# Performance work log

Measured on AMD Instinct MI355X. Metric: run time of the kernel, lower is better.

Reference implementation:

```python
import jax, jax.numpy as jnp
import numpy as np

K = 20           # neighbors
ALPHA = 1.0      # clustering alpha
BN_EPS = 1e-5
NEG_SLOPE = 0.2


def knn_idx(x, k):
    # x: (B, C, N) -> idx (B, N, k) of k nearest neighbors by squared L2
    xx = jnp.sum(x * x, axis=1)                      # (B, N)
    inner = jnp.einsum('bcn,bcm->bnm', x, x)         # (B, N, N)
    pd = -xx[:, :, None] + 2.0 * inner - xx[:, None, :]  # negative sq dist
    return jax.lax.top_k(pd, k)[1]


def graph_feature(x, k):
    # x: (B, C, N) -> (B, 2C, N, k): concat(neighbor - center, center)
    xt = jnp.transpose(x, (0, 2, 1))                 # (B, N, C)
    idx = knn_idx(x, k)                              # (B, N, k)
    feat = jax.vmap(lambda f, i: f[i])(xt, idx)      # (B, N, k, C)
    center = jnp.broadcast_to(xt[:, :, None, :], feat.shape)
    out = jnp.concatenate([feat - center, center], axis=-1)
    return jnp.transpose(out, (0, 3, 1, 2))


def batchnorm(x, g, b, axes):
    # training-mode BN: batch statistics over `axes`, channel axis = 1
    m = jnp.mean(x, axes, keepdims=True)
    v = jnp.var(x, axes, keepdims=True)
    shape = [1] * x.ndim
    shape[1] = x.shape[1]
    return (x - m) / jnp.sqrt(v + BN_EPS) * g.reshape(shape) + b.reshape(shape)


def conv_block2d(x, w, g, b):
    # 1x1 Conv2d (no bias) + BN2d + LeakyReLU; x (B,Cin,N,k), w (Cout,Cin)
    y = jnp.einsum('oc,bcnk->bonk', w, x)
    return jax.nn.leaky_relu(batchnorm(y, g, b, (0, 2, 3)), NEG_SLOPE)


def setup_inputs() -> dict:
    key = jax.random.key(0)
    ks = jax.random.split(key, 16)
    B, C, N = 4, 3, 2048
    d = {
        'x1': jax.random.normal(ks[0], (B, C, N), jnp.float32),
        'x2': jax.random.normal(ks[1], (B, C, N), jnp.float32),
        'w1': jax.random.normal(ks[2], (64, 6), jnp.float32) * 0.1,
        'g1': jnp.ones((64,), jnp.float32), 'b1': jnp.zeros((64,), jnp.float32),
        'w2': jax.random.normal(ks[3], (64, 128), jnp.float32) * 0.1,
        'g2': jnp.ones((64,), jnp.float32), 'b2': jnp.zeros((64,), jnp.float32),
        'w3': jax.random.normal(ks[4], (128, 128), jnp.float32) * 0.1,
        'g3': jnp.ones((128,), jnp.float32), 'b3': jnp.zeros((128,), jnp.float32),
        'w4': jax.random.normal(ks[5], (256, 256), jnp.float32) * 0.1,
        'g4': jnp.ones((256,), jnp.float32), 'b4': jnp.zeros((256,), jnp.float32),
        'w5': jax.random.normal(ks[6], (1024, 512), jnp.float32) * 0.05,
        'g5': jnp.ones((1024,), jnp.float32), 'b5': jnp.zeros((1024,), jnp.float32),
        'lw1': jax.random.normal(ks[7], (256, 2048), jnp.float32) * 0.02,
        'lb1': jnp.zeros((256,), jnp.float32),
        'lw2': jax.random.normal(ks[8], (64, 256), jnp.float32) * 0.05,
        'lb2': jnp.zeros((64,), jnp.float32),
        'lw3': jax.random.normal(ks[9], (10, 64), jnp.float32) * 0.1,
        'lb3': jnp.zeros((10,), jnp.float32),
        'cw': jax.random.normal(ks[10], (800, 10), jnp.float32) * 0.1,
    }
    return d


def reference(x1, x2, w1, g1, b1, w2, g2, b2, w3, g3, b3, w4, g4, b4,
              w5, g5, b5, lw1, lb1, lw2, lb2, lw3, lb3, cw):

    def single(x):
        h = conv_block2d(graph_feature(x, K), w1, g1, b1)
        f1 = h.max(axis=-1)                            # (B,64,N)
        h = conv_block2d(graph_feature(f1, K), w2, g2, b2)
        f2 = h.max(axis=-1)                            # (B,64,N)
        h = conv_block2d(graph_feature(f2, K), w3, g3, b3)
        f3 = h.max(axis=-1)                            # (B,128,N)
        h = conv_block2d(graph_feature(f3, K), w4, g4, b4)
        f4 = h.max(axis=-1)                            # (B,256,N)
        h = jnp.concatenate([f1, f2, f3, f4], axis=1)  # (B,512,N)
        h = jnp.einsum('oc,bcn->bon', w5, h)           # 1x1 Conv1d
        h = jax.nn.leaky_relu(batchnorm(h, g5, b5, (0, 2)), NEG_SLOPE)
        z = jnp.concatenate([h.max(axis=-1), h.mean(axis=-1)], axis=1)  # (B,2048)
        z = z @ lw1.T + lb1
        z = z @ lw2.T + lb2
        e = z @ lw3.T + lb3                            # (B,10)
        diff = e[:, None, :] - cw                      # (B,800,10)
        x_dis = jnp.sum(diff * diff, axis=2)           # (B,800)
        q = (1.0 + x_dis / ALPHA) ** (-(ALPHA + 1.0) / 2.0)
        q = q / jnp.sum(q, axis=1, keepdims=True)
        return q, e, x_dis

    q1, e1, xd1 = single(x1)
    q2, e2, xd2 = single(x2)
    d = e1 - e2 + 1e-6  # torch F.pairwise_distance eps
    sim = jnp.sqrt(jnp.sum(d * d, axis=1))
    return (sim, q1, q2, e1, e2, xd1)
```

## Files before the change

kernel.cpp:

```cpp
#include <hip/hip_runtime.h>
#include <math.h>

#define BB 4
#define NN 2048
#define KK 20
#define NEG 0.2f

#define QOFF0 4
#define QOFF1 3204
#define EOFF0 6404
#define EOFF1 6444
#define XDOFF 6484

typedef unsigned short u16;
typedef unsigned int u32;
typedef __attribute__((ext_vector_type(8))) short s16x8;
typedef __attribute__((ext_vector_type(4))) float f32x4;
typedef __attribute__((ext_vector_type(16))) float f32x16;
typedef __attribute__((ext_vector_type(8))) u16 u16x8;

__device__ __forceinline__ u16 f2bf(float x) {
    u32 u = __float_as_uint(x);
    u += 0x7FFFu + ((u >> 16) & 1u);
    return (u16)(u >> 16);
}

__global__ __launch_bounds__(256) void transpose_x_kernel(
    const float* __restrict__ x, float* __restrict__ fnc, float* __restrict__ xx,
    u16* __restrict__ fh, u16* __restrict__ fl)
{
    int gid = blockIdx.x * 256 + threadIdx.x;
    int b = gid >> 11, n = gid & 2047;
    float s = 0.f;
    float v[3];
#pragma unroll
    for (int c = 0; c < 3; ++c) {
        v[c] = x[((size_t)b * 3 + c) * NN + n];
        fnc[(size_t)gid * 3 + c] = v[c];
        s += v[c] * v[c];
    }
    xx[gid] = s;
    u16x8 z = {0,0,0,0,0,0,0,0};
    u16x8 h0 = z, l0 = z;
#pragma unroll
    for (int c = 0; c < 3; ++c) {
        u16 hb = f2bf(v[c]);
        h0[c] = hb;
        l0[c] = f2bf(v[c] - __uint_as_float((u32)hb << 16));
    }
    u16* fhp = fh + (size_t)gid * 32;
    u16* flp = fl + (size_t)gid * 32;
    *(u16x8*)(fhp)      = h0; *(u16x8*)(fhp + 8)  = z;
    *(u16x8*)(fhp + 16) = z;  *(u16x8*)(fhp + 24) = z;
    *(u16x8*)(flp)      = l0; *(u16x8*)(flp + 8)  = z;
    *(u16x8*)(flp + 16) = z;  *(u16x8*)(flp + 24) = z;
}

__global__ __launch_bounds__(256) void norms_kernel(
    const float* __restrict__ h512, int choff, int C, float* __restrict__ xx)
{
    int gid = blockIdx.x * 256 + threadIdx.x;
    const float* p = h512 + (size_t)gid * 512 + choff;
    float s = 0.f;
    for (int c = 0; c < C; ++c) { float v = p[c]; s += v * v; }
    xx[gid] = s;
}

#define NINFV -3.4e38f

template<int CTRL>
__device__ __forceinline__ void dmax2(float& a1, float& a2)
{
    int b1i = __builtin_amdgcn_update_dpp(
        __float_as_int(a1), __float_as_int(a1), CTRL, 0xf, 0xf, false);
    int b2i = __builtin_amdgcn_update_dpp(
        __float_as_int(a2), __float_as_int(a2), CTRL, 0xf, 0xf, false);
    float b1 = __int_as_float(b1i), b2 = __int_as_float(b2i);
    float n1 = fmaxf(a1, b1);
    float n2 = fmaxf(fminf(a1, b1), fmaxf(a2, b2));
    a1 = n1; a2 = n2;
}

__device__ __forceinline__ void gload_lds16(const void* g, void* l) {
    __builtin_amdgcn_global_load_lds(
        (const __attribute__((address_space(1))) void*)g,
        (__attribute__((address_space(3))) void*)l, 16, 0, 0);
}

template<int KT>
__global__ __launch_bounds__(512) void knn_dotg_kernel(
    const u16* __restrict__ Fh, const u16* __restrict__ Fl,
    int ncs, int choff, int bbase,
    const float* __restrict__ xx, float* __restrict__ S)
{
    __shared__ u16 Bst[8][2][KT][512];
    int tid = threadIdx.x;
    int bid = blockIdx.x;
    int bl  = bid & 1, b = bbase + bl;
    int r0  = (bid >> 1) << 4;
    int wv = tid >> 6, lane = tid & 63;
    int l15 = lane & 15, l4 = lane >> 4;

    const u16* Ah0 = Fh + (size_t)(b * NN + r0 + l15) * ncs + choff + l4 * 8;
    const u16* Al0 = Fl + (size_t)(b * NN + r0 + l15) * ncs + choff + l4 * 8;
    s16x8 a_h[KT], a_l[KT];
#pragma unroll
    for (int kt = 0; kt < KT; ++kt) {
        a_h[kt] = *(const s16x8*)(Ah0 + kt * 32);
        a_l[kt] = *(const s16x8*)(Al0 + kt * 32);
    }

    int srow = lane >> 2;
    int scc  = (lane & 3) ^ (srow & 3);
    const float* xb = xx + b * NN;
    float* Sb = S + (size_t)bl * NN * NN;

    for (int t = 0; t < 16; ++t) {
        int c0 = (t << 7) + (wv << 4);
        size_t srcrow = (size_t)(b * NN + c0 + srow) * ncs + choff;
#pragma unroll
        for (int kt = 0; kt < KT; ++kt) {
            gload_lds16(Fh + srcrow + kt * 32 + scc * 8, &Bst[wv][0][kt][0]);
            gload_lds16(Fl + srcrow + kt * 32 + scc * 8, &Bst[wv][1][kt][0]);
        }
        asm volatile("s_waitcnt vmcnt(0)" ::: "memory");

        f32x4 acc;
#pragma unroll
        for (int i = 0; i < 4; ++i) acc[i] = 0.f;
        int rb = l15 * 32 + ((l4 ^ (l15 & 3)) << 3);
#pragma unroll
        for (int kt = 0; kt < KT; ++kt) {
            s16x8 bh  = *(const s16x8*)&Bst[wv][0][kt][rb];
            s16x8 bl_ = *(const s16x8*)&Bst[wv][1][kt][rb];
            acc = __builtin_amdgcn_mfma_f32_16x16x32_bf16(a_h[kt], bh,  acc, 0, 0, 0);
            acc = __builtin_amdgcn_mfma_f32_16x16x32_bf16(a_l[kt], bh,  acc, 0, 0, 0);
            acc = __builtin_amdgcn_mfma_f32_16x16x32_bf16(a_h[kt], bl_, acc, 0, 0, 0);
        }
        float xv = xb[c0 + l15];
#pragma unroll
        for (int i = 0; i < 4; ++i)
            Sb[(size_t)(r0 + l4 * 4 + i) * NN + c0 + l15] = 2.f * acc[i] - xv;
    }
}

__global__ __launch_bounds__(256) void knn_selg_kernel(
    const float* __restrict__ S, int bbase, int* __restrict__ idxout)
{
    int tid = threadIdx.x;
    int w = tid >> 6, lane = tid & 63;
    int row = blockIdx.x * 4 + w;
    int bl = row >> 11, n = row & 2047;
    const float* sb = S + ((size_t)bl * NN + n) * NN;
    int* op = idxout + ((size_t)((bbase + bl) * NN + n)) * KK;

    float rv[32];
#pragma unroll
    for (int j = 0; j < 32; ++j) {
        float vv = sb[lane + (j << 6)];
        rv[j] = (lane + (j << 6) == n) ? NINFV : vv;
    }
    if (lane == 0) op[0] = n;

    float v1 = NINFV, v2 = NINFV, v3 = NINFV, v4 = NINFV;
    int j1 = -1, j2 = -1, j3 = -1, j4 = -1;
#pragma unroll
    for (int j = 0; j < 32; ++j) {
        float vv = rv[j];
        if (vv > v1) { v4 = v3; j4 = j3; v3 = v2; j3 = j2; v2 = v1; j2 = j1; v1 = vv; j1 = j; }
        else if (vv > v2) { v4 = v3; j4 = j3; v3 = v2; j3 = j2; v2 = vv; j2 = j; }
        else if (vv > v3) { v4 = v3; j4 = j3; v3 = vv; j3 = j; }
        else if (vv > v4) { v4 = vv; j4 = j; }
    }

    unsigned consumed = 0u;

    for (int it = 1; it < KK; it += 2) {
        float r1 = v1, r2 = v2;
        dmax2<0x111>(r1, r2);
        dmax2<0x112>(r1, r2);
        dmax2<0x114>(r1, r2);
        dmax2<0x118>(r1, r2);
        dmax2<0x142>(r1, r2);
        dmax2<0x143>(r1, r2);
        float m1 = __int_as_float(
            __builtin_amdgcn_readlane(__float_as_int(r1), 63));
        float m2 = __int_as_float(
            __builtin_amdgcn_readlane(__float_as_int(r2), 63));
        unsigned long long k1 = __ballot(v1 == m1);
        if (lane == __ffsll(k1) - 1) {
            op[it] = lane + (j1 << 6);
            consumed |= 1u << j1;
            v1 = v2; j1 = j2; v2 = v3; j2 = j3; v3 = v4; j3 = j4;
            v4 = NINFV; j4 = -1;
        }
        if (it + 1 < KK) {
            unsigned long long k2 = __ballot(v1 == m2);
            if (lane == __ffsll(k2) - 1) {
                op[it + 1] = lane + (j1 << 6);
                consumed |= 1u << j1;
                v1 = v2; j1 = j2; v2 = v3; j2 = j3; v3 = v4; j3 = j4;
                v4 = NINFV; j4 = -1;
            }
        }
        if (__any(v2 == NINFV)) {
            if (v2 == NINFV) {
                v1 = NINFV; v2 = NINFV; v3 = NINFV; v4 = NINFV;
                j1 = -1; j2 = -1; j3 = -1; j4 = -1;
#pragma unroll
                for (int j = 0; j < 32; ++j) {
                    if (!(consumed & (1u << j))) {
                        float vv = rv[j];
                        if (vv > v1) { v4 = v3; j4 = j3; v3 = v2; j3 = j2; v2 = v1; j2 = j1; v1 = vv; j1 = j; }
                        else if (vv > v2) { v4 = v3; j4 = j3; v3 = v2; j3 = j2; v2 = vv; j2 = j; }
                        else if (vv > v3) { v4 = v3; j4 = j3; v3 = vv; j3 = j; }
                        else if (vv > v4) { v4 = vv; j4 = j; }
                    }
                }
            }
        }
    }
}

template<int C, int COUT>
__global__ __launch_bounds__(256) void gemm_gh_kernel(
    const float* __restrict__ fnc, int ncs, int choff,
    const float* __restrict__ W,
    float* __restrict__ G, float* __restrict__ H)
{
    constexpr int GROUPS = 256 / COUT;
    constexpr int RPT = 8 / GROUPS;
    __shared__ float Fs[8][C];
    int tid = threadIdx.x;
    int row0 = blockIdx.x * 8;
    for (int i = tid; i < 8 * C; i += 256) {
        int r = i / C, c = i % C;
        Fs[r][c] = fnc[(size_t)(row0 + r) * ncs + choff + c];
    }
    __syncthreads();
    int o = tid % COUT;
    int r0 = (tid / COUT) * RPT;
    float g[RPT], h[RPT];
#pragma unroll
    for (int r = 0; r < RPT; ++r) { g[r] = 0.f; h[r] = 0.f; }
    const float* wr = W + (size_t)o * 2 * C;
    for (int c = 0; c < C; ++c) {
        float w1 = wr[c], wd = wr[C + c] - w1;
#pragma unroll
        for (int r = 0; r < RPT; ++r) {
            float f = Fs[r0 + r][c];
            g[r] += f * w1; h[r] += f * wd;
        }
    }
#pragma unroll
    for (int r = 0; r < RPT; ++r) {
        size_t rr = (size_t)(row0 + r0 + r) * COUT + o;
        G[rr] = g[r]; H[rr] = h[r];
    }
}

template<int COUT>
__global__ __launch_bounds__(256) void gather_kernel(
    const float* __restrict__ G, const float* __restrict__ H,
    const int* __restrict__ idx,
    float* __restrict__ ymax, float* __restrict__ ymin,
    float* __restrict__ psum, float* __restrict__ psumsq)
{
    constexpr int RPI = 256 / COUT;
    constexpr int NITER = 16 / RPI;
    int tid = threadIdx.x;
    int o = tid % COUT;
    int rsub = tid / COUT;
    int row0 = blockIdx.x * 16;
    float s = 0.f, s2 = 0.f;
    for (int it = 0; it < NITER; ++it) {
        int r = row0 + it * RPI + rsub;
        int b = r >> 11;
        float h = H[(size_t)r * COUT + o];
        const int* ip = idx + (size_t)r * KK;
        float mx = -3.4e38f, mn = 3.4e38f;
#pragma unroll
        for (int j = 0; j < KK; ++j) {
            int m = ip[j];
            float g = G[((size_t)(b << 11) + m) * COUT + o];
            float y = g + h;
            mx = fmaxf(mx, y); mn = fminf(mn, y);
            s += y; s2 += y * y;
        }
        ymax[(size_t)r * COUT + o] = mx;
        ymin[(size_t)r * COUT + o] = mn;
    }
    __shared__ float ls[256], ls2[256];
    ls[tid] = s; ls2[tid] = s2;
    __syncthreads();
    for (int st = 128; st >= COUT; st >>= 1) {
        if (tid < st) { ls[tid] += ls[tid + st]; ls2[tid] += ls2[tid + st]; }
        __syncthreads();
    }
    if (tid < COUT) {
        psum[(size_t)blockIdx.x * COUT + tid]   = ls[tid];
        psumsq[(size_t)blockIdx.x * COUT + tid] = ls2[tid];
    }
}

__global__ __launch_bounds__(256) void bnscale_kernel(
    const float* __restrict__ psum, const float* __restrict__ psumsq,
    int nblk, int cout, float cnt,
    const float* __restrict__ gw, const float* __restrict__ bw,
    float* __restrict__ ss)
{
    int o = blockIdx.x;
    int t = threadIdx.x;
    float s = 0.f, s2 = 0.f;
    for (int i = t; i < nblk; i += 256) {
        s  += psum[(size_t)i * cout + o];
        s2 += psumsq[(size_t)i * cout + o];
    }
    __shared__ float ls[256], ls2[256];
    ls[t] = s; ls2[t] = s2;
    __syncthreads();
    for (int st = 128; st > 0; st >>= 1) {
        if (t < st) { ls[t] += ls[t + st]; ls2[t] += ls2[t + st]; }
        __syncthreads();
    }
    if (t == 0) {
        float m = ls[0] / cnt;
        float v = ls2[0] / cnt - m * m;
        float sc = gw[o] / sqrtf(v + 1e-5f);
        float sh = bw[o] - m * sc;
        ss[o * 2] = sc; ss[o * 2 + 1] = sh;
    }
}

__global__ __launch_bounds__(256) void apply_kernel(
    const float* __restrict__ ymax, const float* __restrict__ ymin,
    const float* __restrict__ ss, int coutShift, int choff,
    float* __restrict__ h512, u16* __restrict__ Ah, u16* __restrict__ Al)
{
    size_t gid = (size_t)blockIdx.x * 256 + threadIdx.x;
    int o = (int)(gid & ((1u << coutShift) - 1));
    size_t r = gid >> coutShift;
    float sc = ss[o * 2], sh = ss[o * 2 + 1];
    float v = (sc >= 0.f) ? ymax[gid] : ymin[gid];
    float a = sc * v + sh;
    float act = (a > 0.f) ? a : NEG * a;
    size_t hidx = r * 512 + choff + o;
    h512[hidx] = act;
    u16 hb = f2bf(act);
    Ah[hidx] = hb;
    Al[hidx] = f2bf(act - __uint_as_float((u32)hb << 16));
}

template<int CO>
__global__ __launch_bounds__(256) void apply_t_kernel(
    const float* __restrict__ ymax, const float* __restrict__ ymin,
    const float* __restrict__ ss, int choff,
    float* __restrict__ h512, float* __restrict__ fcn,
    u16* __restrict__ Ah, u16* __restrict__ Al)
{
    constexpr int TILES_O = CO >> 6;
    __shared__ float tile[64][65];
    int tr = blockIdx.x / TILES_O;
    int to = blockIdx.x % TILES_O;
    int r0 = tr * 64, o0 = to * 64;
    int t = threadIdx.x;
    int lr = t >> 6;
    int lo = t & 63;
    int o = o0 + lo;
    float sc = ss[o * 2], sh = ss[o * 2 + 1];
#pragma unroll
    for (int rr = 0; rr < 64; rr += 4) {
        int r = r0 + rr + lr;
        size_t gid = (size_t)r * CO + o;
        float v = (sc >= 0.f) ? ymax[gid] : ymin[gid];
        float a = sc * v + sh;
        float act = (a > 0.f) ? a : NEG * a;
        size_t hidx = (size_t)r * 512 + choff + o;
        h512[hidx] = act;
        u16 hb = f2bf(act);
        Ah[hidx] = hb;
        Al[hidx] = f2bf(act - __uint_as_float((u32)hb << 16));
        tile[rr + lr][lo] = act;
    }
    __syncthreads();
    int b = r0 >> 11;
    int n0 = r0 & 2047;
#pragma unroll
    for (int oo = 0; oo < 64; oo += 4) {
        fcn[((size_t)(b * CO + o0 + oo + lr)) * NN + n0 + lo] = tile[lo][oo + lr];
    }
}

__global__ __launch_bounds__(256) void tobf16_b_kernel(
    const float* __restrict__ Bm, u16* __restrict__ Bh, u16* __restrict__ Bl)
{
    int gid = blockIdx.x * 256 + threadIdx.x;
    size_t off = (size_t)gid * 8;
    float4 v0 = *(const float4*)(Bm + off);
    float4 v1 = *(const float4*)(Bm + off + 4);
    float x[8] = {v0.x, v0.y, v0.z, v0.w, v1.x, v1.y, v1.z, v1.w};
    u16x8 h, l;
#pragma unroll
    for (int j = 0; j < 8; ++j) {
        u16 hb = f2bf(x[j]);
        h[j] = hb;
        l[j] = f2bf(x[j] - __uint_as_float((u32)hb << 16));
    }
    *(u16x8*)(Bh + off) = h;
    *(u16x8*)(Bl + off) = l;
}

__global__ __launch_bounds__(256) void gemm5_mfma_kernel(
    const u16* __restrict__ Ah, const u16* __restrict__ Al,
    const u16* __restrict__ Bh, const u16* __restrict__ Bl,
    float* __restrict__ Y, float* __restrict__ psum, float* __restrict__ psumsq)
{
    __shared__ u16 As[2][128][64];
    __shared__ u16 Bs[2][128][64];
    __shared__ float scs[4][128];
    __shared__ float sqs[4][128];

    int tid = threadIdx.x;
    int bm = blockIdx.x & 63, bn = blockIdx.x >> 6;
    int row0 = bm * 128, col0 = bn * 128;
    int w = tid >> 6, lane = tid & 63;
    int wr = w >> 1, wc = w & 1;

    int isB = w >> 1, plane = w & 1;
    int srow = lane >> 3;
    int kch  = (lane & 7) ^ srow;
    const u16* gbase = isB ? (plane ? Bl : Bh) : (plane ? Al : Ah);
    int rc0 = isB ? col0 : row0;
    const u16* gsrc0 = gbase + (size_t)(rc0 + srow) * 512 + kch * 8;
    u16* lds0 = (isB ? &Bs[0][0][0] : &As[0][0][0]) + plane * 8192;

    f32x16 acc[2][2];
#pragma unroll
    for (int i = 0; i < 2; ++i)
#pragma unroll
        for (int j = 0; j < 2; ++j)
#pragma unroll
            for (int r = 0; r < 16; ++r) acc[i][j][r] = 0.f;

    int ln = lane & 31, l5 = lane >> 5;
    const u16* Afb = &As[0][0][0] + (size_t)(wr * 64 + ln) * 64;
    const u16* Bfb = &Bs[0][0][0] + (size_t)(wc * 64 + ln) * 64;

    for (int k0 = 0; k0 < 512; k0 += 64) {
#pragma unroll
        for (int cc = 0; cc < 16; ++cc)
            gload_lds16(gsrc0 + (size_t)cc * 4096 + k0, lds0 + cc * 512);
        __syncthreads();

#pragma unroll
        for (int ks = 0; ks < 4; ++ks) {
            int pos = ((ks * 2 + l5) ^ (ln & 7)) * 8;
            s16x8 ah0 = *(const s16x8*)(Afb + pos);
            s16x8 ah1 = *(const s16x8*)(Afb + 2048 + pos);
            s16x8 al0 = *(const s16x8*)(Afb + 8192 + pos);
            s16x8 al1 = *(const s16x8*)(Afb + 8192 + 2048 + pos);
#pragma unroll
            for (int j = 0; j < 2; ++j) {
                s16x8 bh = *(const s16x8*)(Bfb + j * 2048 + pos);
                s16x8 bl = *(const s16x8*)(Bfb + 8192 + j * 2048 + pos);
                acc[0][j] = __builtin_amdgcn_mfma_f32_32x32x16_bf16(ah0, bh, acc[0][j], 0, 0, 0);
                acc[1][j] = __builtin_amdgcn_mfma_f32_32x32x16_bf16(ah1, bh, acc[1][j], 0, 0, 0);
                acc[0][j] = __builtin_amdgcn_mfma_f32_32x32x16_bf16(al0, bh, acc[0][j], 0, 0, 0);
                acc[1][j] = __builtin_amdgcn_mfma_f32_32x32x16_bf16(al1, bh, acc[1][j], 0, 0, 0);
                acc[0][j] = __builtin_amdgcn_mfma_f32_32x32x16_bf16(ah0, bl, acc[0][j], 0, 0, 0);
                acc[1][j] = __builtin_amdgcn_mfma_f32_32x32x16_bf16(ah1, bl, acc[1][j], 0, 0, 0);
            }
        }
        __syncthreads();
    }

#pragma unroll
    for (int i = 0; i < 2; ++i)
#pragma unroll
        for (int reg = 0; reg < 16; ++reg) {
            int row = row0 + wr * 64 + i * 32 + l5 * 4 + (reg >> 2) * 8 + (reg & 3);
            float* yp = Y + (size_t)row * 1024 + col0 + wc * 64 + ln;
            yp[0]  = acc[i][0][reg];
            yp[32] = acc[i][1][reg];
        }

#pragma unroll
    for (int j = 0; j < 2; ++j) {
        float s = 0.f, q = 0.f;
#pragma unroll
        for (int i = 0; i < 2; ++i)
#pragma unroll
            for (int reg = 0; reg < 16; ++reg) {
                float v = acc[i][j][reg];
                s += v; q += v * v;
            }
        scs[wr * 2 + l5][wc * 64 + j * 32 + ln] = s;
        sqs[wr * 2 + l5][wc * 64 + j * 32 + ln] = q;
    }
    __syncthreads();
    if (tid < 128) {
        float s = 0.f, q = 0.f;
#pragma unroll
        for (int p = 0; p < 4; ++p) { s += scs[p][tid]; q += sqs[p][tid]; }
        psum[(size_t)bm * 1024 + col0 + tid]   = s;
        psumsq[(size_t)bm * 1024 + col0 + tid] = q;
    }
}

__global__ __launch_bounds__(256) void pool_part_kernel(
    const float* __restrict__ Y, const float* __restrict__ ss,
    float* __restrict__ pmax, float* __restrict__ psum)
{
    int bid = blockIdx.x;
    int b = bid >> 6;
    int n0 = (bid & 63) * 32;
    int t = threadIdx.x;
    int o = t * 4;
    float4 sA = *(const float4*)(ss + o * 2);
    float4 sB = *(const float4*)(ss + o * 2 + 4);
    float4 mx = {-3.4e38f, -3.4e38f, -3.4e38f, -3.4e38f};
    float4 sm = {0.f, 0.f, 0.f, 0.f};
    const float* Yb = Y + ((size_t)b * NN + n0) * 1024 + o;
#pragma unroll 4
    for (int n = 0; n < 32; ++n) {
        float4 v = *(const float4*)(Yb + (size_t)n * 1024);
        float a0 = sA.x * v.x + sA.y; a0 = (a0 > 0.f) ? a0 : NEG * a0;
        float a1 = sA.z * v.y + sA.w; a1 = (a1 > 0.f) ? a1 : NEG * a1;
        float a2 = sB.x * v.z + sB.y; a2 = (a2 > 0.f) ? a2 : NEG * a2;
        float a3 = sB.z * v.w + sB.w; a3 = (a3 > 0.f) ? a3 : NEG * a3;
        mx.x = fmaxf(mx.x, a0); sm.x += a0;
        mx.y = fmaxf(mx.y, a1); sm.y += a1;
        mx.z = fmaxf(mx.z, a2); sm.z += a2;
        mx.w = fmaxf(mx.w, a3); sm.w += a3;
    }
    size_t po = (size_t)bid * 1024 + o;
    *(float4*)(pmax + po) = mx;
    *(float4*)(psum + po) = sm;
}

__global__ __launch_bounds__(256) void pool_comb_kernel(
    const float* __restrict__ pmax, const float* __restrict__ psum,
    float* __restrict__ z)
{
    int b = blockIdx.x;
    int t = threadIdx.x;
    int o = t * 4;
    float4 mx = {-3.4e38f, -3.4e38f, -3.4e38f, -3.4e38f};
    float4 sm = {0.f, 0.f, 0.f, 0.f};
    for (int ch = 0; ch < 64; ++ch) {
        size_t po = ((size_t)(b * 64 + ch)) * 1024 + o;
        float4 m = *(const float4*)(pmax + po);
        float4 s = *(const float4*)(psum + po);
        mx.x = fmaxf(mx.x, m.x); mx.y = fmaxf(mx.y, m.y);
        mx.z = fmaxf(mx.z, m.z); mx.w = fmaxf(mx.w, m.w);
        sm.x += s.x; sm.y += s.y; sm.z += s.z; sm.w += s.w;
    }
    *(float4*)(z + (size_t)b * 2048 + o) = mx;
    float4 mn = {sm.x * (1.f / 2048.f), sm.y * (1.f / 2048.f),
                 sm.z * (1.f / 2048.f), sm.w * (1.f / 2048.f)};
    *(float4*)(z + (size_t)b * 2048 + 1024 + o) = mn;
}

__global__ __launch_bounds__(64) void gemv1_kernel(
    const float* __restrict__ z, const float* __restrict__ lw1,
    const float* __restrict__ lb1, float* __restrict__ z1)
{
    int o = blockIdx.x;
    int lane = threadIdx.x;
    const float* wr = lw1 + (size_t)o * 2048;
    float a0 = 0.f, a1 = 0.f, a2 = 0.f, a3 = 0.f;
    for (int c = lane; c < 2048; c += 64) {
        float w = wr[c];
        a0 += z[c] * w; a1 += z[2048 + c] * w;
        a2 += z[4096 + c] * w; a3 += z[6144 + c] * w;
    }
#pragma unroll
    for (int off = 32; off > 0; off >>= 1) {
        a0 += __shfl_down(a0, off); a1 += __shfl_down(a1, off);
        a2 += __shfl_down(a2, off); a3 += __shfl_down(a3, off);
    }
    if (lane == 0) {
        float bias = lb1[o];
        z1[o] = a0 + bias; z1[256 + o] = a1 + bias;
        z1[512 + o] = a2 + bias; z1[768 + o] = a3 + bias;
    }
}

__global__ __launch_bounds__(1024) void head2_kernel(
    const float* __restrict__ z1,
    const float* __restrict__ lw2, const float* __restrict__ lb2,
    const float* __restrict__ lw3, const float* __restrict__ lb3,
    const float* __restrict__ cw,
    float* __restrict__ out, float* __restrict__ e_store, int which)
{
    __shared__ float z2s[4][64];
    __shared__ float es[4][10];
    __shared__ float qs[3200];
    __shared__ float dnm[4];
    int t = threadIdx.x;
    if (t < 256) {
        int b = t >> 6, o = t & 63;
        float acc = lb2[o];
        const float* wr = lw2 + (size_t)o * 256;
        const float* zr = z1 + b * 256;
        for (int c = 0; c < 256; ++c) acc += zr[c] * wr[c];
        z2s[b][o] = acc;
    }
    __syncthreads();
    if (t < 40) {
        int b = t / 10, o = t % 10;
        float acc = lb3[o];
        const float* wr = lw3 + o * 64;
        for (int c = 0; c < 64; ++c) acc += z2s[b][c] * wr[c];
        es[b][o] = acc;
        int eoff = (which == 0) ? EOFF0 : EOFF1;
        out[eoff + b * 10 + o] = acc;
        e_store[which * 40 + b * 10 + o] = acc;
    }
    __syncthreads();
    for (int p = t; p < 3200; p += 1024) {
        int b = p / 800, j = p % 800;
        float xd = 0.f;
        const float* cwr = cw + j * 10;
#pragma unroll
        for (int i = 0; i < 10; ++i) { float d = es[b][i] - cwr[i]; xd += d * d; }
        qs[p] = 1.0f / (1.0f + xd);
        if (which == 0) out[XDOFF + p] = xd;
    }
    __syncthreads();
    if (t < 4) {
        float s = 0.f;
        for (int j = 0; j < 800; ++j) s += qs[t * 800 + j];
        dnm[t] = s;
    }
    __syncthreads();
    int qoff = (which == 0) ? QOFF0 : QOFF1;
    for (int p = t; p < 3200; p += 1024) out[qoff + p] = qs[p] / dnm[p / 800];
}

__global__ void sim_kernel(const float* __restrict__ e_store, float* __restrict__ out)
{
    int t = threadIdx.x;
    if (t < 4) {
        float s = 0.f;
        for (int i = 0; i < 10; ++i) {
            float d = e_store[t * 10 + i] - e_store[40 + t * 10 + i] + 1e-6f;
            s += d * d;
        }
        out[t] = sqrtf(s);
    }
}

extern "C" void kernel_launch(void* const* d_in, const int* in_sizes, int n_in,
                              void* d_out, int out_size, void* d_ws, size_t ws_size,
                              hipStream_t stream)
{
    const float* x1  = (const float*)d_in[0];
    const float* x2  = (const float*)d_in[1];
    const float* w1  = (const float*)d_in[2];
    const float* g1  = (const float*)d_in[3];
    const float* b1  = (const float*)d_in[4];
    const float* w2  = (const float*)d_in[5];
    const float* g2  = (const float*)d_in[6];
    const float* b2  = (const float*)d_in[7];
    const float* w3  = (const float*)d_in[8];
    const float* g3  = (const float*)d_in[9];
    const float* b3  = (const float*)d_in[10];
    const float* w4  = (const float*)d_in[11];
    const float* g4  = (const float*)d_in[12];
    const float* b4  = (const float*)d_in[13];
    const float* w5  = (const float*)d_in[14];
    const float* g5  = (const float*)d_in[15];
    const float* b5  = (const float*)d_in[16];
    const float* lw1 = (const float*)d_in[17];
    const float* lb1 = (const float*)d_in[18];
    const float* lw2 = (const float*)d_in[19];
    const float* lb2 = (const float*)d_in[20];
    const float* lw3 = (const float*)d_in[21];
    const float* lb3 = (const float*)d_in[22];
    const float* cw  = (const float*)d_in[23];
    float* out = (float*)d_out;

    float* ws   = (float*)d_ws;
    float* h512 = ws;
    float* G    = h512 + 4194304;
    float* Hb   = G + 2097152;
    float* ymax = Hb + 2097152;
    float* ymin = ymax + 2097152;
    float* y5   = G;
    float* Sscr = G;
    float* fcn  = ymin + 2097152;
    float* fnc1 = fcn + 1048576;
    float* xx   = fnc1 + 32768;
    float* psum = xx + 8192;
    float* psq  = psum + 131072;
    float* ss   = psq + 131072;
    float* p5s  = ss + 2048;
    float* p5q  = p5s + 262144;
    float* ss5  = p5q + 262144;
    float* z    = ss5 + 2048;
    float* z1   = z + 8192;
    float* est  = z1 + 1024;
    int*   idx  = (int*)(est + 128);
    u16*   Ahs  = (u16*)(idx + BB * NN * KK);
    u16*   Als  = Ahs + 4194304;
    u16*   Bhs  = Als + 4194304;
    u16*   Bls  = Bhs + 524288;
    u16*   fnc1h = Bls + 524288;
    u16*   fnc1l = fnc1h + 262144;

    tobf16_b_kernel<<<256, 256, 0, stream>>>(w5, Bhs, Bls);

    for (int which = 0; which < 2; ++which) {
        const float* xin = which ? x2 : x1;
        transpose_x_kernel<<<32, 256, 0, stream>>>(xin, fnc1, xx, fnc1h, fnc1l);
        for (int bp = 0; bp < 2; ++bp) {
            knn_dotg_kernel<1><<<256, 512, 0, stream>>>(fnc1h, fnc1l, 32, 0, 2*bp, xx, Sscr);
            knn_selg_kernel<<<1024, 256, 0, stream>>>(Sscr, 2*bp, idx);
        }
        gemm_gh_kernel<3, 64><<<1024, 256, 0, stream>>>(fnc1, 3, 0, w1, G, Hb);
        gather_kernel<64><<<512, 256, 0, stream>>>(G, Hb, idx, ymax, ymin, psum, psq);
        bnscale_kernel<<<64, 256, 0, stream>>>(psum, psq, 512, 64, 163840.f, g1, b1, ss);
        apply_t_kernel<64><<<128, 256, 0, stream>>>(ymax, ymin, ss, 0, h512, fcn, Ahs, Als);
        norms_kernel<<<32, 256, 0, stream>>>(h512, 0, 64, xx);
        for (int bp = 0; bp < 2; ++bp) {
            knn_dotg_kernel<2><<<256, 512, 0, stream>>>(Ahs, Als, 512, 0, 2*bp, xx, Sscr);
            knn_selg_kernel<<<1024, 256, 0, stream>>>(Sscr, 2*bp, idx);
        }
        gemm_gh_kernel<64, 64><<<1024, 256, 0, stream>>>(h512, 512, 0, w2, G, Hb);
        gather_kernel<64><<<512, 256, 0, stream>>>(G, Hb, idx, ymax, ymin, psum, psq);
        bnscale_kernel<<<64, 256, 0, stream>>>(psum, psq, 512, 64, 163840.f, g2, b2, ss);
        apply_t_kernel<64><<<128, 256, 0, stream>>>(ymax, ymin, ss, 64, h512, fcn, Ahs, Als);
        norms_kernel<<<32, 256, 0, stream>>>(h512, 64, 64, xx);
        for (int bp = 0; bp < 2; ++bp) {
            knn_dotg_kernel<2><<<256, 512, 0, stream>>>(Ahs, Als, 512, 64, 2*bp, xx, Sscr);
            knn_selg_kernel<<<1024, 256, 0, stream>>>(Sscr, 2*bp, idx);
        }
        gemm_gh_kernel<64, 128><<<1024, 256, 0, stream>>>(h512, 512, 64, w3, G, Hb);
        gather_kernel<128><<<512, 256, 0, stream>>>(G, Hb, idx, ymax, ymin, psum, psq);
        bnscale_kernel<<<128, 256, 0, stream>>>(psum, psq, 512, 128, 163840.f, g3, b3, ss);
        apply_t_kernel<128><<<256, 256, 0, stream>>>(ymax, ymin, ss, 128, h512, fcn, Ahs, Als);
        norms_kernel<<<32, 256, 0, stream>>>(h512, 128, 128, xx);
        for (int bp = 0; bp < 2; ++bp) {
            knn_dotg_kernel<4><<<256, 512, 0, stream>>>(Ahs, Als, 512, 128, 2*bp, xx, Sscr);
            knn_selg_kernel<<<1024, 256, 0, stream>>>(Sscr, 2*bp, idx);
        }
        gemm_gh_kernel<128, 256><<<1024, 256, 0, stream>>>(h512, 512, 128, w4, G, Hb);
        gather_kernel<256><<<512, 256, 0, stream>>>(G, Hb, idx, ymax, ymin, psum, psq);
        bnscale_kernel<<<256, 256, 0, stream>>>(psum, psq, 512, 256, 163840.f, g4, b4, ss);
        apply_kernel<<<8192, 256, 0, stream>>>(ymax, ymin, ss, 8, 256, h512, Ahs, Als);
        gemm5_mfma_kernel<<<512, 256, 0, stream>>>(Ahs, Als, Bhs, Bls, y5, p5s, p5q);
        bnscale_kernel<<<1024, 256, 0, stream>>>(p5s, p5q, 64, 1024, 8192.f, g5, b5, ss5);
        pool_part_kernel<<<256, 256, 0, stream>>>(y5, ss5, p5s, p5q);
        pool_comb_kernel<<<4, 256, 0, stream>>>(p5s, p5q, z);
        gemv1_kernel<<<256, 64, 0, stream>>>(z, lw1, lb1, z1);
        head2_kernel<<<1, 1024, 0, stream>>>(z1, lw2, lb2, lw3, lb3, cw, out, est, which);
    }
    sim_kernel<<<1, 64, 0, stream>>>(est, out);
}
```

Measured before the change: 1.311 ms.

## Replace scalar edge-conv GH GEMMs with split-bf16 MFMA kernels

Replaces the FP32 scalar per-point GEMMs that compute the center and neighbor-difference projections with a bf16 hi/lo split MFMA kernel using three products per tile to keep near-FP32 accuracy. The weights are pre-split into hi/lo bf16 with padded K once per call, and the already-existing bf16 copies of the features are reused as the A operands. This targets the scalar FMA cost of the four gemm_gh stages. It adds a small weight-conversion prologue and makes the results depend on how accurate the three-term bf16 emulation is.

```diff
diff --git a/kernel.cpp b/kernel.cpp
--- a/kernel.cpp
+++ b/kernel.cpp
@@ -222,40 +222,68 @@
     }
 }
 
-template<int C, int COUT>
-__global__ __launch_bounds__(256) void gemm_gh_kernel(
-    const float* __restrict__ fnc, int ncs, int choff,
-    const float* __restrict__ W,
+__global__ __launch_bounds__(256) void tobf16_w_kernel(
+    const float* __restrict__ W, int C, int COUT, int KP,
+    u16* __restrict__ Wh, u16* __restrict__ Wl)
+{
+    int idx = blockIdx.x * 256 + threadIdx.x;
+    if (idx >= 2 * COUT * KP) return;
+    int row = idx / KP, c = idx - row * KP;
+    int o = (row >= COUT) ? row - COUT : row;
+    float val = 0.f;
+    if (c < C) {
+        float w1 = W[(size_t)o * 2 * C + c];
+        val = (row >= COUT) ? (W[(size_t)o * 2 * C + C + c] - w1) : w1;
+    }
+    u16 hb = f2bf(val);
+    Wh[idx] = hb;
+    Wl[idx] = f2bf(val - __uint_as_float((u32)hb << 16));
+}
+
+template<int KT, int COUT>
+__global__ __launch_bounds__(256) void gemm_gh_mfma_kernel(
+    const u16* __restrict__ Fh, const u16* __restrict__ Fl,
+    int ncs, int choff,
+    const u16* __restrict__ Wh, const u16* __restrict__ Wl,
     float* __restrict__ G, float* __restrict__ H)
 {
-    constexpr int GROUPS = 256 / COUT;
-    constexpr int RPT = 8 / GROUPS;
-    __shared__ float Fs[8][C];
+    constexpr int KP = KT * 32;
+    constexpr int NT = (2 * COUT) >> 4;
     int tid = threadIdx.x;
-    int row0 = blockIdx.x * 8;
-    for (int i = tid; i < 8 * C; i += 256) {
-        int r = i / C, c = i % C;
-        Fs[r][c] = fnc[(size_t)(row0 + r) * ncs + choff + c];
-    }
-    __syncthreads();
-    int o = tid % COUT;
-    int r0 = (tid / COUT) * RPT;
-    float g[RPT], h[RPT];
-#pragma unroll
-    for (int r = 0; r < RPT; ++r) { g[r] = 0.f; h[r] = 0.f; }
-    const float* wr = W + (size_t)o * 2 * C;
-    for (int c = 0; c < C; ++c) {
-        float w1 = wr[c], wd = wr[C + c] - w1;
-#pragma unroll
-        for (int r = 0; r < RPT; ++r) {
-            float f = Fs[r0 + r][c];
-            g[r] += f * w1; h[r] += f * wd;
-        }
-    }
-#pragma unroll
-    for (int r = 0; r < RPT; ++r) {
-        size_t rr = (size_t)(row0 + r0 + r) * COUT + o;
-        G[rr] = g[r]; H[rr] = h[r];
+    int r0 = blockIdx.x << 4;
+    int wv = tid >> 6, lane = tid & 63;
+    int l15 = lane & 15, l4 = lane >> 4;
+
+    const u16* Ah0 = Fh + (size_t)(r0 + l15) * ncs + choff + l4 * 8;
+    const u16* Al0 = Fl + (size_t)(r0 + l15) * ncs + choff + l4 * 8;
+    s16x8 a_h[KT], a_l[KT];
+#pragma unroll
+    for (int kt = 0; kt < KT; ++kt) {
+        a_h[kt] = *(const s16x8*)(Ah0 + kt * 32);
+        a_l[kt] = *(const s16x8*)(Al0 + kt * 32);
+    }
+
+    for (int t = wv; t < NT; t += 4) {
+        int c0 = t << 4;
+        const u16* Bh0 = Wh + (size_t)(c0 + l15) * KP + l4 * 8;
+        const u16* Bl0 = Wl + (size_t)(c0 + l15) * KP + l4 * 8;
+        f32x4 acc;
+#pragma unroll
+        for (int i = 0; i < 4; ++i) acc[i] = 0.f;
+#pragma unroll
+        for (int kt = 0; kt < KT; ++kt) {
+            s16x8 bh = *(const s16x8*)(Bh0 + kt * 32);
+            s16x8 bl = *(const s16x8*)(Bl0 + kt * 32);
+            acc = __builtin_amdgcn_mfma_f32_16x16x32_bf16(a_h[kt], bh, acc, 0, 0, 0);
+            acc = __builtin_amdgcn_mfma_f32_16x16x32_bf16(a_l[kt], bh, acc, 0, 0, 0);
+            acc = __builtin_amdgcn_mfma_f32_16x16x32_bf16(a_h[kt], bl, acc, 0, 0, 0);
+        }
+        int col = c0 + l15;
+        float* dst = (col < COUT) ? G : H;
+        int cc = (col < COUT) ? col : col - COUT;
+#pragma unroll
+        for (int i = 0; i < 4; ++i)
+            dst[(size_t)(r0 + l4 * 4 + i) * COUT + cc] = acc[i];
     }
 }
 
@@ -708,8 +736,14 @@
     u16*   Bls  = Bhs + 524288;
     u16*   fnc1h = Bls + 524288;
     u16*   fnc1l = fnc1h + 262144;
+    u16*   Wh   = fnc1l + 262144;
+    u16*   Wl   = Wh + 98304;
 
     tobf16_b_kernel<<<256, 256, 0, stream>>>(w5, Bhs, Bls);
+    tobf16_w_kernel<<<16,  256, 0, stream>>>(w1, 3,   64,  32,  Wh,         Wl);
+    tobf16_w_kernel<<<32,  256, 0, stream>>>(w2, 64,  64,  64,  Wh + 4096,  Wl + 4096);
+    tobf16_w_kernel<<<64,  256, 0, stream>>>(w3, 64,  128, 64,  Wh + 12288, Wl + 12288);
+    tobf16_w_kernel<<<256, 256, 0, stream>>>(w4, 128, 256, 128, Wh + 28672, Wl + 28672);
 
     for (int which = 0; which < 2; ++which) {
         const float* xin = which ? x2 : x1;
@@ -718,7 +752,7 @@
             knn_dotg_kernel<1><<<256, 512, 0, stream>>>(fnc1h, fnc1l, 32, 0, 2*bp, xx, Sscr);
             knn_selg_kernel<<<1024, 256, 0, stream>>>(Sscr, 2*bp, idx);
         }
-        gemm_gh_kernel<3, 64><<<1024, 256, 0, stream>>>(fnc1, 3, 0, w1, G, Hb);
+        gemm_gh_mfma_kernel<1, 64><<<512, 256, 0, stream>>>(fnc1h, fnc1l, 32, 0, Wh, Wl, G, Hb);
         gather_kernel<64><<<512, 256, 0, stream>>>(G, Hb, idx, ymax, ymin, psum, psq);
         bnscale_kernel<<<64, 256, 0, stream>>>(psum, psq, 512, 64, 163840.f, g1, b1, ss);
         apply_t_kernel<64><<<128, 256, 0, stream>>>(ymax, ymin, ss, 0, h512, fcn, Ahs, Als);
@@ -727,7 +761,7 @@
             knn_dotg_kernel<2><<<256, 512, 0, stream>>>(Ahs, Als, 512, 0, 2*bp, xx, Sscr);
             knn_selg_kernel<<<1024, 256, 0, stream>>>(Sscr, 2*bp, idx);
         }
-        gemm_gh_kernel<64, 64><<<1024, 256, 0, stream>>>(h512, 512, 0, w2, G, Hb);
+        gemm_gh_mfma_kernel<2, 64><<<512, 256, 0, stream>>>(Ahs, Als, 512, 0, Wh + 4096, Wl + 4096, G, Hb);
         gather_kernel<64><<<512, 256, 0, stream>>>(G, Hb, idx, ymax, ymin, psum, psq);
         bnscale_kernel<<<64, 256, 0, stream>>>(psum, psq, 512, 64, 163840.f, g2, b2, ss);
         apply_t_kernel<64><<<128, 256, 0, stream>>>(ymax, ymin, ss, 64, h512, fcn, Ahs, Als);
@@ -736,7 +770,7 @@
             knn_dotg_kernel<2><<<256, 512, 0, stream>>>(Ahs, Als, 512, 64, 2*bp, xx, Sscr);
             knn_selg_kernel<<<1024, 256, 0, stream>>>(Sscr, 2*bp, idx);
         }
-        gemm_gh_kernel<64, 128><<<1024, 256, 0, stream>>>(h512, 512, 64, w3, G, Hb);
+        gemm_gh_mfma_kernel<2, 128><<<512, 256, 0, stream>>>(Ahs, Als, 512, 64, Wh + 12288, Wl + 12288, G, Hb);
         gather_kernel<128><<<512, 256, 0, stream>>>(G, Hb, idx, ymax, ymin, psum, psq);
         bnscale_kernel<<<128, 256, 0, stream>>>(psum, psq, 512, 128, 163840.f, g3, b3, ss);
         apply_t_kernel<128><<<256, 256, 0, stream>>>(ymax, ymin, ss, 128, h512, fcn, Ahs, Als);
@@ -745,7 +779,7 @@
             knn_dotg_kernel<4><<<256, 512, 0, stream>>>(Ahs, Als, 512, 128, 2*bp, xx, Sscr);
             knn_selg_kernel<<<1024, 256, 0, stream>>>(Sscr, 2*bp, idx);
         }
-        gemm_gh_kernel<128, 256><<<1024, 256, 0, stream>>>(h512, 512, 128, w4, G, Hb);
+        gemm_gh_mfma_kernel<4, 256><<<512, 256, 0, stream>>>(Ahs, Als, 512, 128, Wh + 28672, Wl + 28672, G, Hb);
         gather_kernel<256><<<512, 256, 0, stream>>>(G, Hb, idx, ymax, ymin, psum, psq);
         bnscale_kernel<<<256, 256, 0, stream>>>(psum, psq, 512, 256, 163840.f, g4, b4, ss);
         apply_kernel<<<8192, 256, 0, stream>>>(ymax, ymin, ss, 8, 256, h512, Ahs, Als);
```

Result: faster. 1.215 ms (-7.3%).
